# Optimization experiments

Measured on AMD Instinct MI355X. Metric: run time of the kernel, lower is better.

Reference implementation:

```python
import jax, jax.numpy as jnp
import numpy as np

NEG_INF = -1e9  # mask fill value used by the original layer
LEAKY_SLOPE = 0.2


def setup_inputs() -> dict:
    key = jax.random.key(0)
    k1, k2, k3, k4 = jax.random.split(key, 4)
    B, N, D_in = 8, 1024, 256
    H, head_dim = 8, 32  # output_dim=256, concat_heads=True
    node_features = jax.random.normal(k1, (B, N, D_in), dtype=jnp.float32)
    adjacency = jax.random.randint(k2, (B, N, N), 0, 2, dtype=jnp.int32)
    W = jax.random.normal(k3, (H, D_in, head_dim), dtype=jnp.float32) * (1.0 / np.sqrt(D_in))
    a = jax.random.normal(k4, (H, 2 * head_dim), dtype=jnp.float32) * (1.0 / np.sqrt(2 * head_dim))
    bias = jnp.zeros((H * head_dim,), dtype=jnp.float32)
    return {"node_features": node_features, "adjacency": adjacency, "W": W, "a": a, "bias": bias}


def reference(node_features, adjacency, W, a, bias):
    # node_features: (B,N,D_in); adjacency: (B,N,N) in {0,1}
    H, _, hd = W.shape
    # Per-head linear transform: (B,H,N,head_dim)
    Wh = jnp.einsum('bni,hij->bhnj', node_features, W)
    # a @ concat(h_i, h_j) == a1 @ h_i + a2 @ h_j  (avoids O(N^2*2hd) concat)
    a1, a2 = a[:, :hd], a[:, hd:]
    e_i = jnp.einsum('bhnj,hj->bhn', Wh, a1)  # (B,H,N) source term
    e_j = jnp.einsum('bhnj,hj->bhn', Wh, a2)  # (B,H,N) target term
    scores = e_i[:, :, :, None] + e_j[:, :, None, :]  # (B,H,N,N)
    # LeakyReLU(0.2) exactly as ops.maximum(x, 0.2*x)
    scores = jnp.maximum(scores, LEAKY_SLOPE * scores)
    mask = adjacency.astype(scores.dtype)[:, None, :, :]  # (B,1,N,N)
    masked = scores * mask + (1.0 - mask) * NEG_INF
    attn = jax.nn.softmax(masked, axis=-1)  # (B,H,N,N)
    attended = jnp.einsum('bhij,bhjk->bhik', attn, Wh)  # (B,H,N,hd)
    B, _, N, _ = attended.shape
    # concat heads -> (B,N,H*hd); head order matches the python loop concat
    out = attended.transpose(0, 2, 1, 3).reshape(B, N, H * hd)
    out = out + bias
    return jax.nn.relu(out)
```

## Files before the change

kernel.cpp:

```cpp
#include <hip/hip_runtime.h>

#define GAT_B   8
#define GAT_N   1024
#define GAT_DIN 256
#define GAT_H   8
#define GAT_HD  32
#define GAT_LOG2E 1.4426950408889634f

typedef unsigned short gu16;
typedef unsigned int   gu32;
typedef __bf16 bf16x8 __attribute__((ext_vector_type(8)));
typedef __bf16 bf16x4 __attribute__((ext_vector_type(4)));
typedef float  f32x4v __attribute__((ext_vector_type(4)));

#if __has_builtin(__builtin_amdgcn_exp2f)
#define GAT_EXP2(x) __builtin_amdgcn_exp2f(x)
#else
#define GAT_EXP2(x) exp2f(x)
#endif

__device__ __forceinline__ float gb2f(gu16 u) { return __uint_as_float(((gu32)u) << 16); }

__device__ __forceinline__ void gat_detect(const gu16* p, int t, int* sflag) {
    if (t < 64) {
        int e0 = (p[2 * t]     >> 7) & 0xFF;
        int e1 = (p[2 * t + 1] >> 7) & 0xFF;
        unsigned long long m = __ballot((e0 >= 140) || (e1 >= 140));
        if (t == 0) *sflag = (m != 0ULL);
    }
}

__global__ __launch_bounds__(512) void CustomGATLayer_90348932038855_pack(
    const void* __restrict__ Xv, const void* __restrict__ Wv, __bf16* __restrict__ wfg)
{
    __shared__ int sflag;
    const int t = threadIdx.x, h = blockIdx.x;
    gat_detect((const gu16*)Xv, t, &sflag);
    __syncthreads();
    const int fp32 = sflag;

    if (fp32) {
        const float* ws = (const float*)Wv + (size_t)h * 8192;
        #pragma unroll
        for (int q = 0; q < 4; ++q) {
            int idx = q * 2048 + t * 4;
            int i = idx >> 5, k = idx & 31;
            float4 v = *(const float4*)(ws + idx);
            int d = h * 8192 + (((i >> 5) * 32 + k) * 4 + ((i >> 3) & 3)) * 8 + (i & 7);
            wfg[d] = (__bf16)v.x; wfg[d + 32] = (__bf16)v.y;
            wfg[d + 64] = (__bf16)v.z; wfg[d + 96] = (__bf16)v.w;
        }
    } else {
        const gu16* ws = (const gu16*)Wv + (size_t)h * 8192;
        gu16* wo = (gu16*)wfg;
        #pragma unroll
        for (int q = 0; q < 4; ++q) {
            int idx = q * 2048 + t * 4;
            int i = idx >> 5, k = idx & 31;
            ushort4 v = *(const ushort4*)(ws + idx);
            int d = h * 8192 + (((i >> 5) * 32 + k) * 4 + ((i >> 3) & 3)) * 8 + (i & 7);
            wo[d] = v.x; wo[d + 32] = v.y; wo[d + 64] = v.z; wo[d + 96] = v.w;
        }
    }
}

__global__ __launch_bounds__(512) void CustomGATLayer_90348932038855_kernel(
    const void* __restrict__ Xv, const __bf16* __restrict__ wfg, const void* __restrict__ Av,
    __bf16* __restrict__ whb, float* __restrict__ e1, float* __restrict__ e2)
{
    __shared__ __align__(16) __bf16 Xl[16][264];
    __shared__ int sflag;

    const int t = threadIdx.x;
    gat_detect((const gu16*)Xv, t, &sflag);

    const int bt = blockIdx.x;
    const int M0 = bt * 16, b = M0 >> 10, nloc = M0 & 1023;
    const int srow = t >> 5, scol = (t & 31) * 8;
    __syncthreads();
    const int fp32 = sflag;

    if (fp32) {
        const float* xs = (const float*)Xv + ((size_t)(b * GAT_N + nloc + srow)) * GAT_DIN + scol;
        float4 x0 = *(const float4*)(xs);
        float4 x1 = *(const float4*)(xs + 4);
        bf16x8 xv;
        xv[0] = (__bf16)x0.x; xv[1] = (__bf16)x0.y; xv[2] = (__bf16)x0.z; xv[3] = (__bf16)x0.w;
        xv[4] = (__bf16)x1.x; xv[5] = (__bf16)x1.y; xv[6] = (__bf16)x1.z; xv[7] = (__bf16)x1.w;
        *(bf16x8*)&Xl[srow][scol] = xv;
    } else {
        const gu16* xs = (const gu16*)Xv + ((size_t)(b * GAT_N + nloc + srow)) * GAT_DIN + scol;
        *(bf16x8*)&Xl[srow][scol] = *(const bf16x8*)xs;
    }
    __syncthreads();

    const int h = t >> 6, l = t & 63, g = l >> 4, c = l & 15;
    const __bf16* wf = wfg + h * 8192;

    f32x4v acc0 = {0.f, 0.f, 0.f, 0.f};
    f32x4v acc1 = {0.f, 0.f, 0.f, 0.f};
    #pragma unroll
    for (int kc = 0; kc < 8; ++kc) {
        bf16x8 af = *(const bf16x8*)&Xl[c][kc * 32 + 8 * g];
        bf16x8 b0 = *(const bf16x8*)(wf + ((kc * 32 + c) * 4 + g) * 8);
        bf16x8 b1 = *(const bf16x8*)(wf + ((kc * 32 + c + 16) * 4 + g) * 8);
        acc0 = __builtin_amdgcn_mfma_f32_16x16x32_bf16(af, b0, acc0, 0, 0, 0);
        acc1 = __builtin_amdgcn_mfma_f32_16x16x32_bf16(af, b1, acc1, 0, 0, 0);
    }

    const int nb = nloc + 4 * g;
    const int jcc = nb >> 5, kg = (nb >> 3) & 3, e0 = nb & 7;
    const size_t fb = (((size_t)(b * GAT_H + h) * 32 + jcc) * 4 + kg) * 32;
    bf16x4 v0, v1;
    v0[0] = (__bf16)acc0[0]; v0[1] = (__bf16)acc0[1];
    v0[2] = (__bf16)acc0[2]; v0[3] = (__bf16)acc0[3];
    v1[0] = (__bf16)acc1[0]; v1[1] = (__bf16)acc1[1];
    v1[2] = (__bf16)acc1[2]; v1[3] = (__bf16)acc1[3];
    *(bf16x4*)(whb + (fb + c) * 8 + e0)      = v0;
    *(bf16x4*)(whb + (fb + c + 16) * 8 + e0) = v1;

    float a1c, a1c16, a2c, a2c16;
    if (fp32) {
        const float* ap = (const float*)Av + h * 2 * GAT_HD;
        a1c = ap[c] * GAT_LOG2E;      a1c16 = ap[c + 16] * GAT_LOG2E;
        a2c = ap[32 + c] * GAT_LOG2E; a2c16 = ap[48 + c] * GAT_LOG2E;
    } else {
        const gu16* ap = (const gu16*)Av + h * 2 * GAT_HD;
        a1c = gb2f(ap[c]) * GAT_LOG2E;      a1c16 = gb2f(ap[c + 16]) * GAT_LOG2E;
        a2c = gb2f(ap[32 + c]) * GAT_LOG2E; a2c16 = gb2f(ap[48 + c]) * GAT_LOG2E;
    }
    float p1[4], p2[4];
    #pragma unroll
    for (int q = 0; q < 4; ++q) {
        p1[q] = acc0[q] * a1c + acc1[q] * a1c16;
        p2[q] = acc0[q] * a2c + acc1[q] * a2c16;
        #pragma unroll
        for (int mm = 1; mm <= 8; mm <<= 1) {
            p1[q] += __shfl_xor(p1[q], mm);
            p2[q] += __shfl_xor(p2[q], mm);
        }
    }
    if (c == 0) {
        const size_t eb = (size_t)(b * GAT_H + h) * GAT_N + nb;
        #pragma unroll
        for (int q = 0; q < 4; ++q) { e1[eb + q] = p1[q]; e2[eb + q] = p2[q]; }
    }
}

__global__ __launch_bounds__(512) void CustomGATLayer_90348932038855_attn(
    const void* __restrict__ Xv, const int* __restrict__ adj, const void* __restrict__ biasv,
    const __bf16* __restrict__ whb, const float* __restrict__ e1f, const float* __restrict__ e2f,
    float* __restrict__ out)
{
    __shared__ __align__(16) float e2l[GAT_H * GAT_N];
    __shared__ gu32 pkl[16][33];
    __shared__ int sflag;

    const int t = threadIdx.x;
    const int h = t >> 6, l = t & 63, g = l >> 4, c = l & 15;
    const int id = blockIdx.x;
    const int b = id & 7, tile = id >> 3;
    const int i0 = tile * 16;

    gat_detect((const gu16*)Xv, t, &sflag);

    {
        const int prow = t >> 5, pd = t & 31;
        const int* ar = adj + ((size_t)(b * GAT_N + i0 + prow)) * GAT_N + pd * 32;
        gu32 m = 0;
        #pragma unroll
        for (int q = 0; q < 8; ++q) {
            int4 v = *(const int4*)(ar + q * 4);
            m |= (v.x != 0 ? 1u : 0u) << (q * 4);
            m |= (v.y != 0 ? 1u : 0u) << (q * 4 + 1);
            m |= (v.z != 0 ? 1u : 0u) << (q * 4 + 2);
            m |= (v.w != 0 ? 1u : 0u) << (q * 4 + 3);
        }
        pkl[prow][pd] = m;
    }
    {
        const float* s = e2f + (size_t)(b * GAT_H + h) * GAT_N;
        float* d = e2l + h * GAT_N;
        #pragma unroll
        for (int q = 0; q < 4; ++q) {
            int off = (q * 64 + l) * 4;
            *(float4*)(d + off) = *(const float4*)(s + off);
        }
    }
    __syncthreads();
    const int fp32 = sflag;

    const float e1r = e1f[(size_t)(b * GAT_H + h) * GAT_N + i0 + c];
    const __bf16* whr = whb + (size_t)(b * GAT_H + h) * (GAT_N * GAT_HD) + g * 256 + c * 8;
    const float* e2h = e2l + h * GAT_N + 8 * g;

    bf16x8 wA0 = *(const bf16x8*)(whr),        wA1 = *(const bf16x8*)(whr + 128);
    bf16x8 wB0 = *(const bf16x8*)(whr + 1024), wB1 = *(const bf16x8*)(whr + 1152);
    bf16x8 wC0 = *(const bf16x8*)(whr + 2048), wC1 = *(const bf16x8*)(whr + 2176);
    bf16x8 wD0 = *(const bf16x8*)(whr + 3072), wD1 = *(const bf16x8*)(whr + 3200);

    f32x4v acc0 = {0.f, 0.f, 0.f, 0.f};
    f32x4v acc1 = {0.f, 0.f, 0.f, 0.f};
    f32x4v accS = {0.f, 0.f, 0.f, 0.f};
    bf16x8 onesf;
    #pragma unroll
    for (int e = 0; e < 8; ++e) onesf[e] = (__bf16)1.0f;

    float bv0, bv1;
    if (fp32) {
        const float* bp = (const float*)biasv + h * GAT_HD;
        bv0 = bp[c]; bv1 = bp[c + 16];
    } else {
        const gu16* bp = (const gu16*)biasv + h * GAT_HD;
        bv0 = gb2f(bp[c]); bv1 = gb2f(bp[c + 16]);
    }

#define GAT_WCOMP(EV, IDX) {                        \
        float s_ = e1r + (EV);                      \
        s_ = fmaxf(s_, 0.2f * s_);                  \
        s_ = fminf(s_, 86.0f);                      \
        float w_ = GAT_EXP2(s_);                    \
        w_ = (ab & (1u << IDX)) ? w_ : 0.0f;        \
        pf[IDX] = (__bf16)w_; }

    #pragma unroll 4
    for (int jc = 0; jc < 32; ++jc) {
        const bf16x8 w0 = wA0, w1 = wA1;
        wA0 = wB0; wA1 = wB1; wB0 = wC0; wB1 = wC1; wC0 = wD0; wC1 = wD1;
        if (jc < 28) {
            const __bf16* wn = whr + (jc + 4) * 1024;
            wD0 = *(const bf16x8*)wn; wD1 = *(const bf16x8*)(wn + 128);
        }
        const gu32 ab = (pkl[c][jc] >> (8 * g)) & 0xFFu;
        float4 ea = *(const float4*)(e2h + jc * 32);
        float4 eb = *(const float4*)(e2h + jc * 32 + 4);
        bf16x8 pf;
        GAT_WCOMP(ea.x, 0) GAT_WCOMP(ea.y, 1)
        GAT_WCOMP(ea.z, 2) GAT_WCOMP(ea.w, 3)
        GAT_WCOMP(eb.x, 4) GAT_WCOMP(eb.y, 5)
        GAT_WCOMP(eb.z, 6) GAT_WCOMP(eb.w, 7)
        acc0 = __builtin_amdgcn_mfma_f32_16x16x32_bf16(pf, w0, acc0, 0, 0, 0);
        acc1 = __builtin_amdgcn_mfma_f32_16x16x32_bf16(pf, w1, acc1, 0, 0, 0);
        accS = __builtin_amdgcn_mfma_f32_16x16x32_bf16(pf, onesf, accS, 0, 0, 0);
    }
#undef GAT_WCOMP

    float* ob = out + (size_t)(b * GAT_N + i0) * (GAT_H * GAT_HD) + h * GAT_HD + c;
    #pragma unroll
    for (int q = 0; q < 4; ++q) {
        float d = accS[q];
        float r = (d > 0.f) ? (1.0f / d) : 0.0f;
        float o0 = fmaxf(acc0[q] * r + bv0, 0.f);
        float o1 = fmaxf(acc1[q] * r + bv1, 0.f);
        ob[(size_t)(4 * g + q) * (GAT_H * GAT_HD)]      = o0;
        ob[(size_t)(4 * g + q) * (GAT_H * GAT_HD) + 16] = o1;
    }
}

extern "C" void kernel_launch(void* const* d_in, const int* in_sizes, int n_in,
                              void* d_out, int out_size, void* d_ws, size_t ws_size,
                              hipStream_t stream) {
    const void* X    = d_in[0];
    const int*  adj  = (const int*)d_in[1];
    const void* Wm   = d_in[2];
    const void* Av   = d_in[3];
    const void* bias = d_in[4];
    float* outp = (float*)d_out;

    __bf16* whb = (__bf16*)d_ws;
    float* e1  = (float*)(whb + (size_t)GAT_B * GAT_H * GAT_N * GAT_HD);
    float* e2  = e1 + (size_t)GAT_B * GAT_H * GAT_N;
    __bf16* wfg = (__bf16*)(e2 + (size_t)GAT_B * GAT_H * GAT_N);

    CustomGATLayer_90348932038855_pack
        <<<dim3(8), 512, 0, stream>>>(X, Wm, wfg);
    CustomGATLayer_90348932038855_kernel
        <<<dim3(512), 512, 0, stream>>>(X, wfg, Av, whb, e1, e2);
    CustomGATLayer_90348932038855_attn
        <<<dim3((GAT_N / 16) * GAT_B), 512, 0, stream>>>(
            X, adj, bias, whb, e1, e2, outp);
}
```

Measured before the change: 121.2 us.

## Split attention key range across two wave groups and pack adjacency with ballots

The attention kernel now launches 1024 threads per block. Two groups of eight waves each cover half of the key/neighbour range for every head, and their partial numerators and denominators are merged through shared memory before normalising and writing the output. The adjacency bitmask is built with one wavefront ballot per 64 columns instead of per-thread int4 scans and bit shifts. This targets latency and occupancy in the serial 32-step MFMA loop, at the cost of an extra LDS reduction, two more barriers, and a launch bound that may squeeze registers.

```diff
diff --git a/kernel.cpp b/kernel.cpp
--- a/kernel.cpp
+++ b/kernel.cpp
@@ -9,6 +9,7 @@
 
 typedef unsigned short gu16;
 typedef unsigned int   gu32;
+typedef unsigned long long gu64;
 typedef __bf16 bf16x8 __attribute__((ext_vector_type(8)));
 typedef __bf16 bf16x4 __attribute__((ext_vector_type(4)));
 typedef float  f32x4v __attribute__((ext_vector_type(4)));
@@ -147,17 +148,18 @@
     }
 }
 
-__global__ __launch_bounds__(512) void CustomGATLayer_90348932038855_attn(
+__global__ __launch_bounds__(1024, 8) void CustomGATLayer_90348932038855_attn(
     const void* __restrict__ Xv, const int* __restrict__ adj, const void* __restrict__ biasv,
     const __bf16* __restrict__ whb, const float* __restrict__ e1f, const float* __restrict__ e2f,
     float* __restrict__ out)
 {
-    __shared__ __align__(16) float e2l[GAT_H * GAT_N];
-    __shared__ gu32 pkl[16][33];
+    __shared__ __align__(16) float e2l[GAT_H][1024];
+    __shared__ gu64 pklu[16][17];
     __shared__ int sflag;
 
     const int t = threadIdx.x;
-    const int h = t >> 6, l = t & 63, g = l >> 4, c = l & 15;
+    const int w = t >> 6, l = t & 63, g = l >> 4, c = l & 15;
+    const int h = w & 7, jh = w >> 3;
     const int id = blockIdx.x;
     const int b = id & 7, tile = id >> 3;
     const int i0 = tile * 16;
@@ -165,24 +167,19 @@
     gat_detect((const gu16*)Xv, t, &sflag);
 
     {
-        const int prow = t >> 5, pd = t & 31;
-        const int* ar = adj + ((size_t)(b * GAT_N + i0 + prow)) * GAT_N + pd * 32;
-        gu32 m = 0;
-        #pragma unroll
-        for (int q = 0; q < 8; ++q) {
-            int4 v = *(const int4*)(ar + q * 4);
-            m |= (v.x != 0 ? 1u : 0u) << (q * 4);
-            m |= (v.y != 0 ? 1u : 0u) << (q * 4 + 1);
-            m |= (v.z != 0 ? 1u : 0u) << (q * 4 + 2);
-            m |= (v.w != 0 ? 1u : 0u) << (q * 4 + 3);
-        }
-        pkl[prow][pd] = m;
+        const int* ar = adj + ((size_t)(b * GAT_N + i0 + w)) * GAT_N;
+        #pragma unroll
+        for (int s = 0; s < 16; ++s) {
+            int v = ar[s * 64 + l];
+            gu64 m = __ballot(v != 0);
+            if (l == 0) pklu[w][s] = m;
+        }
     }
     {
-        const float* s = e2f + (size_t)(b * GAT_H + h) * GAT_N;
-        float* d = e2l + h * GAT_N;
-        #pragma unroll
-        for (int q = 0; q < 4; ++q) {
+        const float* s = e2f + (size_t)(b * GAT_H + h) * GAT_N + jh * 512;
+        float* d = &e2l[h][jh * 512];
+        #pragma unroll
+        for (int q = 0; q < 2; ++q) {
             int off = (q * 64 + l) * 4;
             *(float4*)(d + off) = *(const float4*)(s + off);
         }
@@ -191,8 +188,10 @@
     const int fp32 = sflag;
 
     const float e1r = e1f[(size_t)(b * GAT_H + h) * GAT_N + i0 + c];
-    const __bf16* whr = whb + (size_t)(b * GAT_H + h) * (GAT_N * GAT_HD) + g * 256 + c * 8;
-    const float* e2h = e2l + h * GAT_N + 8 * g;
+    const __bf16* whr = whb + (size_t)(b * GAT_H + h) * (GAT_N * GAT_HD)
+                            + jh * 16384 + g * 256 + c * 8;
+    const float* e2h = &e2l[h][jh * 512 + 8 * g];
+    const gu32* pkr = (const gu32*)pklu[c] + jh * 16;
 
     bf16x8 wA0 = *(const bf16x8*)(whr),        wA1 = *(const bf16x8*)(whr + 128);
     bf16x8 wB0 = *(const bf16x8*)(whr + 1024), wB1 = *(const bf16x8*)(whr + 1152);
@@ -205,15 +204,6 @@
     bf16x8 onesf;
     #pragma unroll
     for (int e = 0; e < 8; ++e) onesf[e] = (__bf16)1.0f;
-
-    float bv0, bv1;
-    if (fp32) {
-        const float* bp = (const float*)biasv + h * GAT_HD;
-        bv0 = bp[c]; bv1 = bp[c + 16];
-    } else {
-        const gu16* bp = (const gu16*)biasv + h * GAT_HD;
-        bv0 = gb2f(bp[c]); bv1 = gb2f(bp[c + 16]);
-    }
 
 #define GAT_WCOMP(EV, IDX) {                        \
         float s_ = e1r + (EV);                      \
@@ -224,14 +214,14 @@
         pf[IDX] = (__bf16)w_; }
 
     #pragma unroll 4
-    for (int jc = 0; jc < 32; ++jc) {
+    for (int jc = 0; jc < 16; ++jc) {
         const bf16x8 w0 = wA0, w1 = wA1;
         wA0 = wB0; wA1 = wB1; wB0 = wC0; wB1 = wC1; wC0 = wD0; wC1 = wD1;
-        if (jc < 28) {
+        if (jc < 12) {
             const __bf16* wn = whr + (jc + 4) * 1024;
             wD0 = *(const bf16x8*)wn; wD1 = *(const bf16x8*)(wn + 128);
         }
-        const gu32 ab = (pkl[c][jc] >> (8 * g)) & 0xFFu;
+        const gu32 ab = (pkr[jc] >> (8 * g)) & 0xFFu;
         float4 ea = *(const float4*)(e2h + jc * 32);
         float4 eb = *(const float4*)(e2h + jc * 32 + 4);
         bf16x8 pf;
@@ -245,15 +235,40 @@
     }
 #undef GAT_WCOMP
 
-    float* ob = out + (size_t)(b * GAT_N + i0) * (GAT_H * GAT_HD) + h * GAT_HD + c;
-    #pragma unroll
-    for (int q = 0; q < 4; ++q) {
-        float d = accS[q];
-        float r = (d > 0.f) ? (1.0f / d) : 0.0f;
-        float o0 = fmaxf(acc0[q] * r + bv0, 0.f);
-        float o1 = fmaxf(acc1[q] * r + bv1, 0.f);
-        ob[(size_t)(4 * g + q) * (GAT_H * GAT_HD)]      = o0;
-        ob[(size_t)(4 * g + q) * (GAT_H * GAT_HD) + 16] = o1;
+    __syncthreads();
+    float4* sc = (float4*)e2l;
+    const int slot = h * 64 + l;
+    if (jh == 1) {
+        sc[slot]        = make_float4(acc0[0], acc0[1], acc0[2], acc0[3]);
+        sc[512 + slot]  = make_float4(acc1[0], acc1[1], acc1[2], acc1[3]);
+        sc[1024 + slot] = make_float4(accS[0], accS[1], accS[2], accS[3]);
+    }
+    __syncthreads();
+    if (jh == 0) {
+        float4 q0 = sc[slot], q1 = sc[512 + slot], q2 = sc[1024 + slot];
+        acc0[0] += q0.x; acc0[1] += q0.y; acc0[2] += q0.z; acc0[3] += q0.w;
+        acc1[0] += q1.x; acc1[1] += q1.y; acc1[2] += q1.z; acc1[3] += q1.w;
+        accS[0] += q2.x; accS[1] += q2.y; accS[2] += q2.z; accS[3] += q2.w;
+
+        float bv0, bv1;
+        if (fp32) {
+            const float* bp = (const float*)biasv + h * GAT_HD;
+            bv0 = bp[c]; bv1 = bp[c + 16];
+        } else {
+            const gu16* bp = (const gu16*)biasv + h * GAT_HD;
+            bv0 = gb2f(bp[c]); bv1 = gb2f(bp[c + 16]);
+        }
+
+        float* ob = out + (size_t)(b * GAT_N + i0) * (GAT_H * GAT_HD) + h * GAT_HD + c;
+        #pragma unroll
+        for (int q = 0; q < 4; ++q) {
+            float d = accS[q];
+            float r = (d > 0.f) ? (1.0f / d) : 0.0f;
+            float o0 = fmaxf(acc0[q] * r + bv0, 0.f);
+            float o1 = fmaxf(acc1[q] * r + bv1, 0.f);
+            ob[(size_t)(4 * g + q) * (GAT_H * GAT_HD)]      = o0;
+            ob[(size_t)(4 * g + q) * (GAT_H * GAT_HD) + 16] = o1;
+        }
     }
 }
 
@@ -268,8 +283,8 @@
     float* outp = (float*)d_out;
 
     __bf16* whb = (__bf16*)d_ws;
-    float* e1  = (float*)(whb + (size_t)GAT_B * GAT_H * GAT_N * GAT_HD);
-    float* e2  = e1 + (size_t)GAT_B * GAT_H * GAT_N;
+    float* e1   = (float*)(whb + (size_t)GAT_B * GAT_H * GAT_N * GAT_HD);
+    float* e2   = e1 + (size_t)GAT_B * GAT_H * GAT_N;
     __bf16* wfg = (__bf16*)(e2 + (size_t)GAT_B * GAT_H * GAT_N);
 
     CustomGATLayer_90348932038855_pack
@@ -277,6 +292,6 @@
     CustomGATLayer_90348932038855_kernel
         <<<dim3(512), 512, 0, stream>>>(X, wfg, Av, whb, e1, e2);
     CustomGATLayer_90348932038855_attn
-        <<<dim3((GAT_N / 16) * GAT_B), 512, 0, stream>>>(
+        <<<dim3((GAT_N / 16) * GAT_B), 1024, 0, stream>>>(
             X, adj, bias, whb, e1, e2, outp);
 }
```

New measurement: 191.8 us. +58.2%, slower.
